# Kernel optimization log

Hardware: AMD Instinct MI355X
Metric: run time of the kernel (lower is better)

Reference implementation:

```python
import jax, jax.numpy as jnp
import numpy as np
from jax.ops import segment_sum

N_NODES = 200_000
N_EDGES = 6_400_000


def gcn_conv(x, W, b, src, dst, num_nodes):
    """PyG GCNConv (default): h = x @ W; add self-loops; symmetric norm; scatter-add; + bias."""
    h = x @ W  # [N, F_out]
    loop = jnp.arange(num_nodes, dtype=src.dtype)
    s = jnp.concatenate([src, loop])  # source (message sender)
    d = jnp.concatenate([dst, loop])  # target (aggregation index)
    ones = jnp.ones(s.shape[0], dtype=h.dtype)
    deg = segment_sum(ones, d, num_segments=num_nodes)  # in-degree incl. self-loop
    dinv = jnp.where(deg > 0, jax.lax.rsqrt(deg), 0.0)
    norm = dinv[s] * dinv[d]  # [E+N]
    msg = h[s] * norm[:, None]  # [E+N, F_out]
    out = segment_sum(msg, d, num_segments=num_nodes)
    return out + b


def setup_inputs() -> dict:
    key = jax.random.key(0)
    ks = jax.random.split(key, 6)
    x = jax.random.normal(ks[0], (N_NODES, 6), dtype=jnp.float32)
    edge_index = jax.random.randint(ks[1], (2, N_EDGES), 0, N_NODES, dtype=jnp.int32)
    W1 = jax.random.normal(ks[2], (6, 16), dtype=jnp.float32) * (1.0 / np.sqrt(6))
    b1 = jnp.zeros((16,), dtype=jnp.float32)
    W2 = jax.random.normal(ks[3], (16, 8), dtype=jnp.float32) * (1.0 / np.sqrt(16))
    b2 = jnp.zeros((8,), dtype=jnp.float32)
    Wfc = jax.random.normal(ks[4], (8, 1), dtype=jnp.float32) * (1.0 / np.sqrt(8))
    bfc = jnp.zeros((1,), dtype=jnp.float32)
    return {"x": x, "edge_index": edge_index, "W1": W1, "b1": b1,
            "W2": W2, "b2": b2, "Wfc": Wfc, "bfc": bfc}


def reference(x, edge_index, W1, b1, W2, b2, Wfc, bfc):
    src, dst = edge_index[0], edge_index[1]
    h = gcn_conv(x, W1, b1, src, dst, N_NODES)
    h = jax.nn.relu(h)
    h = gcn_conv(h, W2, b2, src, dst, N_NODES)
    h = jax.nn.relu(h)
    out = h @ Wfc + bfc
    return jax.nn.sigmoid(out)
```

## Files before the change

kernel.cpp:

```cpp
#include <hip/hip_runtime.h>
#include <math.h>


#define TPB 256
#define NBS 8
#define NBKT 256
#define MAXB 1024
#define BPT (MAXB / TPB)
#define CHUNK 4096
#define EPT (CHUNK / TPB)
#define CAP 9216
#define RPT (CAP / TPB)

__device__ __forceinline__ unsigned short f2bf(float f) {
    unsigned u = __float_as_uint(f);
    unsigned r = (u + 0x7FFFu + ((u >> 16) & 1u)) >> 16;
    return (unsigned short)r;
}
__device__ __forceinline__ unsigned pk2(float a, float b) {
    return (unsigned)f2bf(a) | ((unsigned)f2bf(b) << 16);
}
#define BFLO(u) __uint_as_float((u) << 16)
#define BFHI(u) __uint_as_float((u) & 0xFFFF0000u)

__global__ void __launch_bounds__(TPB) k_fb1(
        const int* __restrict__ dst, int* __restrict__ C, int e, int nb) {
    __shared__ int h[MAXB];
    int t = threadIdx.x;
    int c0 = blockIdx.x * CHUNK;
    int csize = min(e - c0, CHUNK);
#pragma unroll
    for (int k = 0; k < BPT; k++) h[t * BPT + k] = 0;
    __syncthreads();
    for (int i = c0 + t; i < c0 + csize; i += TPB)
        atomicAdd(&h[dst[i] >> NBS], 1);
    __syncthreads();
    int* row = C + (size_t)blockIdx.x * nb;
    for (int b = t; b < nb; b += TPB) row[b] = h[b];
}

__global__ void __launch_bounds__(TPB) k_scanC(
        const int* __restrict__ C, int* __restrict__ O, int* __restrict__ btot,
        int nchunk, int nb) {
    __shared__ int sm[TPB];
    int b = blockIdx.x, t = threadIdx.x;
    int run = b * CAP;
    for (int c0 = 0; c0 < nchunk; c0 += TPB) {
        int c = c0 + t;
        int v = (c < nchunk) ? C[(size_t)c * nb + b] : 0;
        sm[t] = v;
        __syncthreads();
        for (int off = 1; off < TPB; off <<= 1) {
            int a = (t >= off) ? sm[t - off] : 0;
            __syncthreads();
            sm[t] += a;
            __syncthreads();
        }
        if (c < nchunk) O[(size_t)c * nb + b] = run + sm[t] - v;
        int tile = sm[TPB - 1];
        __syncthreads();
        run += tile;
    }
    if (t == 0) btot[b] = run - b * CAP;
}

__global__ void __launch_bounds__(TPB) k_fillbin(
        const int* __restrict__ src, const int* __restrict__ dst,
        const int* __restrict__ O, int* __restrict__ binned, int e, int nb) {
    __shared__ int stage[CHUNK];
    __shared__ unsigned short bs[CHUNK];
    __shared__ int h[MAXB];
    __shared__ int excl[MAXB];
    __shared__ int delta[MAXB];
    __shared__ int tmp[TPB];
    int t = threadIdx.x;
    int c0 = blockIdx.x * CHUNK;
    int csize = min(e - c0, CHUNK);
#pragma unroll
    for (int k = 0; k < BPT; k++) h[t * BPT + k] = 0;
    __syncthreads();
    int dreg[EPT];
#pragma unroll
    for (int k = 0; k < EPT; k++) {
        int idx = t + k * TPB;
        int d = (idx < csize) ? dst[c0 + idx] : -1;
        dreg[k] = d;
        if (d >= 0) atomicAdd(&h[d >> NBS], 1);
    }
    __syncthreads();
    int loc[BPT];
    int ts = 0;
#pragma unroll
    for (int k = 0; k < BPT; k++) { loc[k] = ts; ts += h[t * BPT + k]; }
    tmp[t] = ts;
    __syncthreads();
    for (int off = 1; off < TPB; off <<= 1) {
        int a = (t >= off) ? tmp[t - off] : 0;
        __syncthreads();
        tmp[t] += a;
        __syncthreads();
    }
    int tbase = tmp[t] - ts;
#pragma unroll
    for (int k = 0; k < BPT; k++) excl[t * BPT + k] = tbase + loc[k];
    __syncthreads();
    const int* Orow = O + (size_t)blockIdx.x * nb;
#pragma unroll
    for (int k = 0; k < BPT; k++) {
        int b = t * BPT + k;
        delta[b] = ((b < nb) ? Orow[b] : 0) - excl[b];
    }
#pragma unroll
    for (int k = 0; k < BPT; k++) { int b = t * BPT + k; h[b] = excl[b]; }
    __syncthreads();
#pragma unroll
    for (int k = 0; k < EPT; k++) {
        int idx = t + k * TPB;
        if (idx < csize) {
            int d = dreg[k];
            int s = src[c0 + idx];
            int b = d >> NBS;
            int r = atomicAdd(&h[b], 1);
            stage[r] = ((d & (NBKT - 1)) << 18) | s;
            bs[r] = (unsigned short)b;
        }
    }
    __syncthreads();
    for (int k = t; k < csize; k += TPB)
        binned[delta[bs[k]] + k] = stage[k];
}

__global__ void __launch_bounds__(TPB) k_sort(
        const int* __restrict__ binned, const int* __restrict__ btot,
        const float* __restrict__ x, int* __restrict__ csr,
        int* __restrict__ rowptr, int* __restrict__ rowend,
        float* __restrict__ dinv, uint4* __restrict__ xdq, int n) {
    __shared__ int stage[CAP];
    __shared__ int cnt[NBKT];
    __shared__ int excl[NBKT];
    __shared__ int curs[NBKT];
    int b = blockIdx.x, t = threadIdx.x;
    int base = b * CAP;
    int c = btot[b];
    cnt[t] = 0;
    __syncthreads();
    int w[RPT];
#pragma unroll
    for (int k = 0; k < RPT; k++) {
        int idx = t + k * TPB;
        w[k] = (idx < c) ? binned[base + idx] : -1;
        if (w[k] >= 0) atomicAdd(&cnt[w[k] >> 18], 1);
    }
    __syncthreads();
    int v = cnt[t];
    excl[t] = v;
    __syncthreads();
    for (int off = 1; off < NBKT; off <<= 1) {
        int a = (t >= off) ? excl[t - off] : 0;
        __syncthreads();
        excl[t] += a;
        __syncthreads();
    }
    int ex = excl[t] - v;
    curs[t] = ex;
    int i = (b << NBS) + t;
    rowptr[i] = base + ex;
    rowend[i] = base + ex + v;
    if (i < n) {
        float di = rsqrtf((float)(v + 1));
        dinv[i] = di;
        uint4 q;
        q.x = pk2(x[i * 6 + 0] * di, x[i * 6 + 1] * di);
        q.y = pk2(x[i * 6 + 2] * di, x[i * 6 + 3] * di);
        q.z = pk2(x[i * 6 + 4] * di, x[i * 6 + 5] * di);
        q.w = 0;
        xdq[i] = q;
    }
    __syncthreads();
#pragma unroll
    for (int k = 0; k < RPT; k++) {
        if (w[k] >= 0) {
            int r = atomicAdd(&curs[w[k] >> 18], 1);
            stage[r] = w[k] & 0x3FFFF;
        }
    }
    __syncthreads();
    for (int k = t; k < c; k += TPB)
        csr[base + k] = stage[k];
}

__global__ void __launch_bounds__(TPB) k_gat1(
        const uint4* __restrict__ xdq, const int* __restrict__ csr,
        const int* __restrict__ rowptr, const int* __restrict__ rowend,
        const float* __restrict__ dinv,
        const float* __restrict__ b1, const float* __restrict__ W1,
        const float* __restrict__ W2, uint2* __restrict__ g2q, int n) {
    __shared__ float w1[96];
    __shared__ float w2[128];
    __shared__ float bb[16];
    if (threadIdx.x < 96) w1[threadIdx.x] = W1[threadIdx.x];
    if (threadIdx.x < 128) w2[threadIdx.x] = W2[threadIdx.x];
    if (threadIdx.x < 16) bb[threadIdx.x] = b1[threadIdx.x];
    __syncthreads();
    int sub = threadIdx.x & 15;
    int i = blockIdx.x * 16 + (threadIdx.x >> 4);
    bool valid = (i < n);
    int r0 = rowptr[i], r1 = rowend[i];
    float a0 = 0.f, a1 = 0.f, a2 = 0.f, a3 = 0.f, a4 = 0.f, a5 = 0.f;
    float c0 = 0.f, c1 = 0.f, c2 = 0.f, c3 = 0.f, c4 = 0.f, c5 = 0.f;
    if (valid && sub == 0) {
        uint4 q = xdq[i];
        a0 += BFLO(q.x); a1 += BFHI(q.x);
        a2 += BFLO(q.y); a3 += BFHI(q.y);
        a4 += BFLO(q.z); a5 += BFHI(q.z);
    }
    int j = r0 + sub;
    while (j + 16 < r1) {
        uint4 q = xdq[csr[j]];
        uint4 p = xdq[csr[j + 16]];
        a0 += BFLO(q.x); a1 += BFHI(q.x);
        a2 += BFLO(q.y); a3 += BFHI(q.y);
        a4 += BFLO(q.z); a5 += BFHI(q.z);
        c0 += BFLO(p.x); c1 += BFHI(p.x);
        c2 += BFLO(p.y); c3 += BFHI(p.y);
        c4 += BFLO(p.z); c5 += BFHI(p.z);
        j += 32;
    }
    if (j < r1) {
        uint4 q = xdq[csr[j]];
        a0 += BFLO(q.x); a1 += BFHI(q.x);
        a2 += BFLO(q.y); a3 += BFHI(q.y);
        a4 += BFLO(q.z); a5 += BFHI(q.z);
    }
    a0 += c0; a1 += c1; a2 += c2; a3 += c3; a4 += c4; a5 += c5;
#pragma unroll
    for (int m = 1; m <= 8; m <<= 1) {
        a0 += __shfl_xor(a0, m); a1 += __shfl_xor(a1, m);
        a2 += __shfl_xor(a2, m); a3 += __shfl_xor(a3, m);
        a4 += __shfl_xor(a4, m); a5 += __shfl_xor(a5, m);
    }
    float di = valid ? dinv[i] : 0.f;
    int f = sub;
    float hf = a0 * w1[f] + a1 * w1[16 + f] + a2 * w1[32 + f]
             + a3 * w1[48 + f] + a4 * w1[64 + f] + a5 * w1[80 + f];
    float tf = fmaxf(di * hf + bb[f], 0.0f);
    float p0 = tf * w2[f * 8 + 0], p1 = tf * w2[f * 8 + 1];
    float p2 = tf * w2[f * 8 + 2], p3 = tf * w2[f * 8 + 3];
    float p4 = tf * w2[f * 8 + 4], p5 = tf * w2[f * 8 + 5];
    float p6 = tf * w2[f * 8 + 6], p7 = tf * w2[f * 8 + 7];
#pragma unroll
    for (int m = 1; m <= 8; m <<= 1) {
        p0 += __shfl_xor(p0, m); p1 += __shfl_xor(p1, m);
        p2 += __shfl_xor(p2, m); p3 += __shfl_xor(p3, m);
        p4 += __shfl_xor(p4, m); p5 += __shfl_xor(p5, m);
        p6 += __shfl_xor(p6, m); p7 += __shfl_xor(p7, m);
    }
    if (valid && sub < 2) {
        float q0 = sub ? p4 : p0, q1 = sub ? p5 : p1;
        float q2 = sub ? p6 : p2, q3 = sub ? p7 : p3;
        uint2 o;
        o.x = pk2(q0 * di, q1 * di);
        o.y = pk2(q2 * di, q3 * di);
        g2q[i * 2 + sub] = o;
    }
}

__global__ void __launch_bounds__(TPB) k_gat2(
        const uint4* __restrict__ g2q, const int* __restrict__ csr,
        const int* __restrict__ rowptr, const int* __restrict__ rowend,
        const float* __restrict__ dinv,
        const float* __restrict__ b2, const float* __restrict__ Wfc,
        const float* __restrict__ bfc, float* __restrict__ out, int n) {
    __shared__ float w[8];
    __shared__ float bb[8];
    __shared__ float bf;
    if (threadIdx.x < 8) { w[threadIdx.x] = Wfc[threadIdx.x]; bb[threadIdx.x] = b2[threadIdx.x]; }
    if (threadIdx.x == 0) bf = bfc[0];
    __syncthreads();
    int sub = threadIdx.x & 15;
    int i = blockIdx.x * 16 + (threadIdx.x >> 4);
    bool valid = (i < n);
    int r0 = rowptr[i], r1 = rowend[i];
    float a0 = 0.f, a1 = 0.f, a2 = 0.f, a3 = 0.f;
    float a4 = 0.f, a5 = 0.f, a6 = 0.f, a7 = 0.f;
    if (valid && sub == 0) {
        uint4 q = g2q[i];
        a0 += BFLO(q.x); a1 += BFHI(q.x); a2 += BFLO(q.y); a3 += BFHI(q.y);
        a4 += BFLO(q.z); a5 += BFHI(q.z); a6 += BFLO(q.w); a7 += BFHI(q.w);
    }
    float c0 = 0.f, c1 = 0.f, c2 = 0.f, c3 = 0.f;
    float c4 = 0.f, c5 = 0.f, c6 = 0.f, c7 = 0.f;
    int j = r0 + sub;
    while (j + 16 < r1) {
        uint4 q = g2q[csr[j]];
        uint4 p = g2q[csr[j + 16]];
        a0 += BFLO(q.x); a1 += BFHI(q.x); a2 += BFLO(q.y); a3 += BFHI(q.y);
        a4 += BFLO(q.z); a5 += BFHI(q.z); a6 += BFLO(q.w); a7 += BFHI(q.w);
        c0 += BFLO(p.x); c1 += BFHI(p.x); c2 += BFLO(p.y); c3 += BFHI(p.y);
        c4 += BFLO(p.z); c5 += BFHI(p.z); c6 += BFLO(p.w); c7 += BFHI(p.w);
        j += 32;
    }
    if (j < r1) {
        uint4 q = g2q[csr[j]];
        a0 += BFLO(q.x); a1 += BFHI(q.x); a2 += BFLO(q.y); a3 += BFHI(q.y);
        a4 += BFLO(q.z); a5 += BFHI(q.z); a6 += BFLO(q.w); a7 += BFHI(q.w);
    }
    a0 += c0; a1 += c1; a2 += c2; a3 += c3;
    a4 += c4; a5 += c5; a6 += c6; a7 += c7;
#pragma unroll
    for (int m = 1; m <= 8; m <<= 1) {
        a0 += __shfl_xor(a0, m); a1 += __shfl_xor(a1, m);
        a2 += __shfl_xor(a2, m); a3 += __shfl_xor(a3, m);
        a4 += __shfl_xor(a4, m); a5 += __shfl_xor(a5, m);
        a6 += __shfl_xor(a6, m); a7 += __shfl_xor(a7, m);
    }
    if (valid && sub == 0) {
        float di = dinv[i];
        float o = bf;
        o += fmaxf(di * a0 + bb[0], 0.0f) * w[0];
        o += fmaxf(di * a1 + bb[1], 0.0f) * w[1];
        o += fmaxf(di * a2 + bb[2], 0.0f) * w[2];
        o += fmaxf(di * a3 + bb[3], 0.0f) * w[3];
        o += fmaxf(di * a4 + bb[4], 0.0f) * w[4];
        o += fmaxf(di * a5 + bb[5], 0.0f) * w[5];
        o += fmaxf(di * a6 + bb[6], 0.0f) * w[6];
        o += fmaxf(di * a7 + bb[7], 0.0f) * w[7];
        out[i] = 1.0f / (1.0f + expf(-o));
    }
}

extern "C" void kernel_launch(void* const* d_in, const int* in_sizes, int n_in,
                              void* d_out, int out_size, void* d_ws, size_t ws_size,
                              hipStream_t stream) {
    const float* x   = (const float*)d_in[0];
    const int*   ei  = (const int*)d_in[1];
    const float* W1  = (const float*)d_in[2];
    const float* b1  = (const float*)d_in[3];
    const float* W2  = (const float*)d_in[4];
    const float* b2  = (const float*)d_in[5];
    const float* Wfc = (const float*)d_in[6];
    const float* bfc = (const float*)d_in[7];
    float* out = (float*)d_out;

    const int n = in_sizes[0] / 6;
    const int e = in_sizes[1] / 2;
    const int* src = ei;
    const int* dst = ei + e;
    const int nb = (n + NBKT - 1) >> NBS;
    const size_t np = (size_t)nb << NBS;
    const int nblk = (e + CHUNK - 1) / CHUNK;
    const size_t reg = (size_t)nb * CAP;

    int* C      = (int*)d_ws;
    int* O      = C + (size_t)nblk * nb;
    int* btot   = O + (size_t)nblk * nb;
    int* binned = btot + MAXB;
    int* csr    = binned + reg;
    int* rowptr = csr + reg;
    int* rowend = rowptr + np;
    float* dinv = (float*)(rowend + np);
    uint4* xdq  = (uint4*)(dinv + np);
    uint2* g2q  = (uint2*)(xdq + np);

    int gw = (n + 15) / 16;

    k_fb1<<<nblk, TPB, 0, stream>>>(dst, C, e, nb);
    k_scanC<<<nb, TPB, 0, stream>>>(C, O, btot, nblk, nb);
    k_fillbin<<<nblk, TPB, 0, stream>>>(src, dst, O, binned, e, nb);
    k_sort<<<nb, TPB, 0, stream>>>(binned, btot, x, csr, rowptr, rowend, dinv, xdq, n);
    k_gat1<<<gw, TPB, 0, stream>>>(xdq, csr, rowptr, rowend, dinv, b1, W1, W2, g2q, n);
    k_gat2<<<gw, TPB, 0, stream>>>((const uint4*)g2q, csr, rowptr, rowend, dinv, b2, Wfc, bfc, out, n);
}
```

Baseline: 277.0 us.

## Replace CSR sort and row gathers with per-bucket shared-memory atomic aggregation

Drops the in-bucket counting sort that built CSR rows. Each layer now aggregates straight from the coarse-binned edge list into per-bucket shared-memory accumulators using float atomics, and one thread per node finishes the dense math (the two 16-lane groups collapse into per-thread loops). This removes the csr/rowptr writes and reads and the sort pass. In exchange it uses many LDS float atomics that can contend on high-degree nodes, launches only nb (~782) blocks of 512 threads, and makes float summation order nondeterministic.

```diff
diff --git a/kernel.cpp b/kernel.cpp
--- a/kernel.cpp
+++ b/kernel.cpp
@@ -3,6 +3,7 @@
 
 
 #define TPB 256
+#define ATPB 512
 #define NBS 8
 #define NBKT 256
 #define MAXB 1024
@@ -10,7 +11,6 @@
 #define CHUNK 4096
 #define EPT (CHUNK / TPB)
 #define CAP 9216
-#define RPT (CAP / TPB)
 
 __device__ __forceinline__ unsigned short f2bf(float f) {
     unsigned u = __float_as_uint(f);
@@ -130,202 +130,139 @@
         binned[delta[bs[k]] + k] = stage[k];
 }
 
-__global__ void __launch_bounds__(TPB) k_sort(
+__global__ void __launch_bounds__(ATPB) k_degxdq(
         const int* __restrict__ binned, const int* __restrict__ btot,
-        const float* __restrict__ x, int* __restrict__ csr,
-        int* __restrict__ rowptr, int* __restrict__ rowend,
-        float* __restrict__ dinv, uint4* __restrict__ xdq, int n) {
-    __shared__ int stage[CAP];
+        const float* __restrict__ x, float* __restrict__ dinv,
+        uint4* __restrict__ xdq, int n) {
     __shared__ int cnt[NBKT];
-    __shared__ int excl[NBKT];
-    __shared__ int curs[NBKT];
     int b = blockIdx.x, t = threadIdx.x;
+    if (t < NBKT) cnt[t] = 0;
+    __syncthreads();
     int base = b * CAP;
     int c = btot[b];
-    cnt[t] = 0;
-    __syncthreads();
-    int w[RPT];
-#pragma unroll
-    for (int k = 0; k < RPT; k++) {
-        int idx = t + k * TPB;
-        w[k] = (idx < c) ? binned[base + idx] : -1;
-        if (w[k] >= 0) atomicAdd(&cnt[w[k] >> 18], 1);
-    }
-    __syncthreads();
-    int v = cnt[t];
-    excl[t] = v;
-    __syncthreads();
-    for (int off = 1; off < NBKT; off <<= 1) {
-        int a = (t >= off) ? excl[t - off] : 0;
-        __syncthreads();
-        excl[t] += a;
-        __syncthreads();
-    }
-    int ex = excl[t] - v;
-    curs[t] = ex;
-    int i = (b << NBS) + t;
-    rowptr[i] = base + ex;
-    rowend[i] = base + ex + v;
-    if (i < n) {
-        float di = rsqrtf((float)(v + 1));
-        dinv[i] = di;
-        uint4 q;
-        q.x = pk2(x[i * 6 + 0] * di, x[i * 6 + 1] * di);
-        q.y = pk2(x[i * 6 + 2] * di, x[i * 6 + 3] * di);
-        q.z = pk2(x[i * 6 + 4] * di, x[i * 6 + 5] * di);
-        q.w = 0;
-        xdq[i] = q;
-    }
-    __syncthreads();
-#pragma unroll
-    for (int k = 0; k < RPT; k++) {
-        if (w[k] >= 0) {
-            int r = atomicAdd(&curs[w[k] >> 18], 1);
-            stage[r] = w[k] & 0x3FFFF;
-        }
-    }
-    __syncthreads();
-    for (int k = t; k < c; k += TPB)
-        csr[base + k] = stage[k];
-}
-
-__global__ void __launch_bounds__(TPB) k_gat1(
-        const uint4* __restrict__ xdq, const int* __restrict__ csr,
-        const int* __restrict__ rowptr, const int* __restrict__ rowend,
-        const float* __restrict__ dinv,
+    for (int j = base + t; j < base + c; j += ATPB)
+        atomicAdd(&cnt[binned[j] >> 18], 1);
+    __syncthreads();
+    if (t < NBKT) {
+        int i = (b << NBS) + t;
+        if (i < n) {
+            float di = rsqrtf((float)(cnt[t] + 1));
+            dinv[i] = di;
+            uint4 q;
+            q.x = pk2(x[i * 6 + 0] * di, x[i * 6 + 1] * di);
+            q.y = pk2(x[i * 6 + 2] * di, x[i * 6 + 3] * di);
+            q.z = pk2(x[i * 6 + 4] * di, x[i * 6 + 5] * di);
+            q.w = 0;
+            xdq[i] = q;
+        }
+    }
+}
+
+__global__ void __launch_bounds__(ATPB) k_agg1(
+        const int* __restrict__ binned, const int* __restrict__ btot,
+        const uint4* __restrict__ xdq, const float* __restrict__ dinv,
         const float* __restrict__ b1, const float* __restrict__ W1,
-        const float* __restrict__ W2, uint2* __restrict__ g2q, int n) {
+        const float* __restrict__ W2, uint4* __restrict__ g2q, int n) {
+    __shared__ float acc[NBKT * 9];
     __shared__ float w1[96];
     __shared__ float w2[128];
     __shared__ float bb[16];
-    if (threadIdx.x < 96) w1[threadIdx.x] = W1[threadIdx.x];
-    if (threadIdx.x < 128) w2[threadIdx.x] = W2[threadIdx.x];
-    if (threadIdx.x < 16) bb[threadIdx.x] = b1[threadIdx.x];
-    __syncthreads();
-    int sub = threadIdx.x & 15;
-    int i = blockIdx.x * 16 + (threadIdx.x >> 4);
-    bool valid = (i < n);
-    int r0 = rowptr[i], r1 = rowend[i];
-    float a0 = 0.f, a1 = 0.f, a2 = 0.f, a3 = 0.f, a4 = 0.f, a5 = 0.f;
-    float c0 = 0.f, c1 = 0.f, c2 = 0.f, c3 = 0.f, c4 = 0.f, c5 = 0.f;
-    if (valid && sub == 0) {
-        uint4 q = xdq[i];
-        a0 += BFLO(q.x); a1 += BFHI(q.x);
-        a2 += BFLO(q.y); a3 += BFHI(q.y);
-        a4 += BFLO(q.z); a5 += BFHI(q.z);
-    }
-    int j = r0 + sub;
-    while (j + 16 < r1) {
-        uint4 q = xdq[csr[j]];
-        uint4 p = xdq[csr[j + 16]];
-        a0 += BFLO(q.x); a1 += BFHI(q.x);
-        a2 += BFLO(q.y); a3 += BFHI(q.y);
-        a4 += BFLO(q.z); a5 += BFHI(q.z);
-        c0 += BFLO(p.x); c1 += BFHI(p.x);
-        c2 += BFLO(p.y); c3 += BFHI(p.y);
-        c4 += BFLO(p.z); c5 += BFHI(p.z);
-        j += 32;
-    }
-    if (j < r1) {
-        uint4 q = xdq[csr[j]];
-        a0 += BFLO(q.x); a1 += BFHI(q.x);
-        a2 += BFLO(q.y); a3 += BFHI(q.y);
-        a4 += BFLO(q.z); a5 += BFHI(q.z);
-    }
-    a0 += c0; a1 += c1; a2 += c2; a3 += c3; a4 += c4; a5 += c5;
-#pragma unroll
-    for (int m = 1; m <= 8; m <<= 1) {
-        a0 += __shfl_xor(a0, m); a1 += __shfl_xor(a1, m);
-        a2 += __shfl_xor(a2, m); a3 += __shfl_xor(a3, m);
-        a4 += __shfl_xor(a4, m); a5 += __shfl_xor(a5, m);
-    }
-    float di = valid ? dinv[i] : 0.f;
-    int f = sub;
-    float hf = a0 * w1[f] + a1 * w1[16 + f] + a2 * w1[32 + f]
-             + a3 * w1[48 + f] + a4 * w1[64 + f] + a5 * w1[80 + f];
-    float tf = fmaxf(di * hf + bb[f], 0.0f);
-    float p0 = tf * w2[f * 8 + 0], p1 = tf * w2[f * 8 + 1];
-    float p2 = tf * w2[f * 8 + 2], p3 = tf * w2[f * 8 + 3];
-    float p4 = tf * w2[f * 8 + 4], p5 = tf * w2[f * 8 + 5];
-    float p6 = tf * w2[f * 8 + 6], p7 = tf * w2[f * 8 + 7];
-#pragma unroll
-    for (int m = 1; m <= 8; m <<= 1) {
-        p0 += __shfl_xor(p0, m); p1 += __shfl_xor(p1, m);
-        p2 += __shfl_xor(p2, m); p3 += __shfl_xor(p3, m);
-        p4 += __shfl_xor(p4, m); p5 += __shfl_xor(p5, m);
-        p6 += __shfl_xor(p6, m); p7 += __shfl_xor(p7, m);
-    }
-    if (valid && sub < 2) {
-        float q0 = sub ? p4 : p0, q1 = sub ? p5 : p1;
-        float q2 = sub ? p6 : p2, q3 = sub ? p7 : p3;
-        uint2 o;
-        o.x = pk2(q0 * di, q1 * di);
-        o.y = pk2(q2 * di, q3 * di);
-        g2q[i * 2 + sub] = o;
-    }
-}
-
-__global__ void __launch_bounds__(TPB) k_gat2(
-        const uint4* __restrict__ g2q, const int* __restrict__ csr,
-        const int* __restrict__ rowptr, const int* __restrict__ rowend,
-        const float* __restrict__ dinv,
+    int t = threadIdx.x;
+    if (t < 96) w1[t] = W1[t];
+    if (t >= 128 && t < 256) w2[t - 128] = W2[t - 128];
+    if (t >= 256 && t < 272) bb[t - 256] = b1[t - 256];
+    for (int k = t; k < NBKT * 9; k += ATPB) acc[k] = 0.0f;
+    __syncthreads();
+    int b = blockIdx.x;
+    int base = b * CAP;
+    int c = btot[b];
+    for (int j = base + t; j < base + c; j += ATPB) {
+        int p = binned[j];
+        uint4 q = xdq[p & 0x3FFFF];
+        float* ap = &acc[(p >> 18) * 9];
+        atomicAdd(ap + 0, BFLO(q.x)); atomicAdd(ap + 1, BFHI(q.x));
+        atomicAdd(ap + 2, BFLO(q.y)); atomicAdd(ap + 3, BFHI(q.y));
+        atomicAdd(ap + 4, BFLO(q.z)); atomicAdd(ap + 5, BFHI(q.z));
+    }
+    __syncthreads();
+    if (t < NBKT) {
+        int i = (b << NBS) + t;
+        if (i < n) {
+            float di = dinv[i];
+            uint4 s = xdq[i];
+            float a0 = acc[t * 9 + 0] + BFLO(s.x);
+            float a1 = acc[t * 9 + 1] + BFHI(s.x);
+            float a2 = acc[t * 9 + 2] + BFLO(s.y);
+            float a3 = acc[t * 9 + 3] + BFHI(s.y);
+            float a4 = acc[t * 9 + 4] + BFLO(s.z);
+            float a5 = acc[t * 9 + 5] + BFHI(s.z);
+            float tf[16];
+#pragma unroll
+            for (int f = 0; f < 16; f++) {
+                float hf = a0 * w1[f] + a1 * w1[16 + f] + a2 * w1[32 + f]
+                         + a3 * w1[48 + f] + a4 * w1[64 + f] + a5 * w1[80 + f];
+                tf[f] = fmaxf(di * hf + bb[f], 0.0f);
+            }
+            float g[8];
+#pragma unroll
+            for (int f2 = 0; f2 < 8; f2++) {
+                float h = 0.0f;
+#pragma unroll
+                for (int f = 0; f < 16; f++) h += tf[f] * w2[f * 8 + f2];
+                g[f2] = h * di;
+            }
+            uint4 o;
+            o.x = pk2(g[0], g[1]); o.y = pk2(g[2], g[3]);
+            o.z = pk2(g[4], g[5]); o.w = pk2(g[6], g[7]);
+            g2q[i] = o;
+        }
+    }
+}
+
+__global__ void __launch_bounds__(ATPB) k_agg2(
+        const int* __restrict__ binned, const int* __restrict__ btot,
+        const uint4* __restrict__ g2q, const float* __restrict__ dinv,
         const float* __restrict__ b2, const float* __restrict__ Wfc,
         const float* __restrict__ bfc, float* __restrict__ out, int n) {
+    __shared__ float acc[NBKT * 9];
     __shared__ float w[8];
     __shared__ float bb[8];
     __shared__ float bf;
-    if (threadIdx.x < 8) { w[threadIdx.x] = Wfc[threadIdx.x]; bb[threadIdx.x] = b2[threadIdx.x]; }
-    if (threadIdx.x == 0) bf = bfc[0];
-    __syncthreads();
-    int sub = threadIdx.x & 15;
-    int i = blockIdx.x * 16 + (threadIdx.x >> 4);
-    bool valid = (i < n);
-    int r0 = rowptr[i], r1 = rowend[i];
-    float a0 = 0.f, a1 = 0.f, a2 = 0.f, a3 = 0.f;
-    float a4 = 0.f, a5 = 0.f, a6 = 0.f, a7 = 0.f;
-    if (valid && sub == 0) {
-        uint4 q = g2q[i];
-        a0 += BFLO(q.x); a1 += BFHI(q.x); a2 += BFLO(q.y); a3 += BFHI(q.y);
-        a4 += BFLO(q.z); a5 += BFHI(q.z); a6 += BFLO(q.w); a7 += BFHI(q.w);
-    }
-    float c0 = 0.f, c1 = 0.f, c2 = 0.f, c3 = 0.f;
-    float c4 = 0.f, c5 = 0.f, c6 = 0.f, c7 = 0.f;
-    int j = r0 + sub;
-    while (j + 16 < r1) {
-        uint4 q = g2q[csr[j]];
-        uint4 p = g2q[csr[j + 16]];
-        a0 += BFLO(q.x); a1 += BFHI(q.x); a2 += BFLO(q.y); a3 += BFHI(q.y);
-        a4 += BFLO(q.z); a5 += BFHI(q.z); a6 += BFLO(q.w); a7 += BFHI(q.w);
-        c0 += BFLO(p.x); c1 += BFHI(p.x); c2 += BFLO(p.y); c3 += BFHI(p.y);
-        c4 += BFLO(p.z); c5 += BFHI(p.z); c6 += BFLO(p.w); c7 += BFHI(p.w);
-        j += 32;
-    }
-    if (j < r1) {
-        uint4 q = g2q[csr[j]];
-        a0 += BFLO(q.x); a1 += BFHI(q.x); a2 += BFLO(q.y); a3 += BFHI(q.y);
-        a4 += BFLO(q.z); a5 += BFHI(q.z); a6 += BFLO(q.w); a7 += BFHI(q.w);
-    }
-    a0 += c0; a1 += c1; a2 += c2; a3 += c3;
-    a4 += c4; a5 += c5; a6 += c6; a7 += c7;
-#pragma unroll
-    for (int m = 1; m <= 8; m <<= 1) {
-        a0 += __shfl_xor(a0, m); a1 += __shfl_xor(a1, m);
-        a2 += __shfl_xor(a2, m); a3 += __shfl_xor(a3, m);
-        a4 += __shfl_xor(a4, m); a5 += __shfl_xor(a5, m);
-        a6 += __shfl_xor(a6, m); a7 += __shfl_xor(a7, m);
-    }
-    if (valid && sub == 0) {
-        float di = dinv[i];
-        float o = bf;
-        o += fmaxf(di * a0 + bb[0], 0.0f) * w[0];
-        o += fmaxf(di * a1 + bb[1], 0.0f) * w[1];
-        o += fmaxf(di * a2 + bb[2], 0.0f) * w[2];
-        o += fmaxf(di * a3 + bb[3], 0.0f) * w[3];
-        o += fmaxf(di * a4 + bb[4], 0.0f) * w[4];
-        o += fmaxf(di * a5 + bb[5], 0.0f) * w[5];
-        o += fmaxf(di * a6 + bb[6], 0.0f) * w[6];
-        o += fmaxf(di * a7 + bb[7], 0.0f) * w[7];
-        out[i] = 1.0f / (1.0f + expf(-o));
+    int t = threadIdx.x;
+    if (t < 8) w[t] = Wfc[t];
+    if (t >= 64 && t < 72) bb[t - 64] = b2[t - 64];
+    if (t == 128) bf = bfc[0];
+    for (int k = t; k < NBKT * 9; k += ATPB) acc[k] = 0.0f;
+    __syncthreads();
+    int b = blockIdx.x;
+    int base = b * CAP;
+    int c = btot[b];
+    for (int j = base + t; j < base + c; j += ATPB) {
+        int p = binned[j];
+        uint4 q = g2q[p & 0x3FFFF];
+        float* ap = &acc[(p >> 18) * 9];
+        atomicAdd(ap + 0, BFLO(q.x)); atomicAdd(ap + 1, BFHI(q.x));
+        atomicAdd(ap + 2, BFLO(q.y)); atomicAdd(ap + 3, BFHI(q.y));
+        atomicAdd(ap + 4, BFLO(q.z)); atomicAdd(ap + 5, BFHI(q.z));
+        atomicAdd(ap + 6, BFLO(q.w)); atomicAdd(ap + 7, BFHI(q.w));
+    }
+    __syncthreads();
+    if (t < NBKT) {
+        int i = (b << NBS) + t;
+        if (i < n) {
+            float di = dinv[i];
+            uint4 s = g2q[i];
+            float o = bf;
+            o += fmaxf(di * (acc[t * 9 + 0] + BFLO(s.x)) + bb[0], 0.0f) * w[0];
+            o += fmaxf(di * (acc[t * 9 + 1] + BFHI(s.x)) + bb[1], 0.0f) * w[1];
+            o += fmaxf(di * (acc[t * 9 + 2] + BFLO(s.y)) + bb[2], 0.0f) * w[2];
+            o += fmaxf(di * (acc[t * 9 + 3] + BFHI(s.y)) + bb[3], 0.0f) * w[3];
+            o += fmaxf(di * (acc[t * 9 + 4] + BFLO(s.z)) + bb[4], 0.0f) * w[4];
+            o += fmaxf(di * (acc[t * 9 + 5] + BFHI(s.z)) + bb[5], 0.0f) * w[5];
+            o += fmaxf(di * (acc[t * 9 + 6] + BFLO(s.w)) + bb[6], 0.0f) * w[6];
+            o += fmaxf(di * (acc[t * 9 + 7] + BFHI(s.w)) + bb[7], 0.0f) * w[7];
+            out[i] = 1.0f / (1.0f + expf(-o));
+        }
     }
 }
 
@@ -355,19 +292,14 @@
     int* O      = C + (size_t)nblk * nb;
     int* btot   = O + (size_t)nblk * nb;
     int* binned = btot + MAXB;
-    int* csr    = binned + reg;
-    int* rowptr = csr + reg;
-    int* rowend = rowptr + np;
-    float* dinv = (float*)(rowend + np);
+    float* dinv = (float*)(binned + reg);
     uint4* xdq  = (uint4*)(dinv + np);
-    uint2* g2q  = (uint2*)(xdq + np);
-
-    int gw = (n + 15) / 16;
+    uint4* g2q  = xdq + np;
 
     k_fb1<<<nblk, TPB, 0, stream>>>(dst, C, e, nb);
     k_scanC<<<nb, TPB, 0, stream>>>(C, O, btot, nblk, nb);
     k_fillbin<<<nblk, TPB, 0, stream>>>(src, dst, O, binned, e, nb);
-    k_sort<<<nb, TPB, 0, stream>>>(binned, btot, x, csr, rowptr, rowend, dinv, xdq, n);
-    k_gat1<<<gw, TPB, 0, stream>>>(xdq, csr, rowptr, rowend, dinv, b1, W1, W2, g2q, n);
-    k_gat2<<<gw, TPB, 0, stream>>>((const uint4*)g2q, csr, rowptr, rowend, dinv, b2, Wfc, bfc, out, n);
-}
+    k_degxdq<<<nb, ATPB, 0, stream>>>(binned, btot, x, dinv, xdq, n);
+    k_agg1<<<nb, ATPB, 0, stream>>>(binned, btot, xdq, dinv, b1, W1, W2, g2q, n);
+    k_agg2<<<nb, ATPB, 0, stream>>>(binned, btot, g2q, dinv, b2, Wfc, bfc, out, n);
+}
```

Measured after the change: 764.2 us. 2.76x slower.
